# Kernel optimization log

Hardware: AMD Instinct MI355X
Metric: run time of the kernel (lower is better)

Reference implementation:

```python
import jax, jax.numpy as jnp
import numpy as np

DIM = 1024
HEADS = 16
DIM_HEAD = 64
SCALE = DIM_HEAD ** -0.5
LN_EPS = 1e-5


def layer_norm(x, g, b):
    mu = jnp.mean(x, axis=-1, keepdims=True)
    var = jnp.mean(jnp.square(x - mu), axis=-1, keepdims=True)
    return (x - mu) * jax.lax.rsqrt(var + LN_EPS) * g + b


def setup_inputs() -> dict:
    key = jax.random.key(0)
    ks = jax.random.split(key, 8)
    w_std = DIM ** -0.5  # keep GEMM outputs O(1)
    return {
        "query": jax.random.normal(ks[0], (4, 512, DIM), jnp.float32),
        "kv": jax.random.normal(ks[1], (4, 2048, DIM), jnp.float32),
        "ln_q_g": jnp.ones((DIM,), jnp.float32),
        "ln_q_b": jnp.zeros((DIM,), jnp.float32),
        "ln_kv_g": jnp.ones((DIM,), jnp.float32),
        "ln_kv_b": jnp.zeros((DIM,), jnp.float32),
        "Wq": jax.random.normal(ks[2], (DIM, DIM), jnp.float32) * w_std,
        "bq": jnp.zeros((DIM,), jnp.float32),
        "Wk": jax.random.normal(ks[3], (DIM, DIM), jnp.float32) * w_std,
        "bk": jnp.zeros((DIM,), jnp.float32),
        "Wv": jax.random.normal(ks[4], (DIM, DIM), jnp.float32) * w_std,
        "bv": jnp.zeros((DIM,), jnp.float32),
        "Wo": jax.random.normal(ks[5], (DIM, DIM), jnp.float32) * w_std,
        "bo": jnp.zeros((DIM,), jnp.float32),
    }


def reference(query, kv, ln_q_g, ln_q_b, ln_kv_g, ln_kv_b,
              Wq, bq, Wk, bk, Wv, bv, Wo, bo):
    kv_n = layer_norm(kv, ln_kv_g, ln_kv_b)            # (b, n_kv, d)
    residual = query
    q_n = layer_norm(query, ln_q_g, ln_q_b)            # (b, n_q, d)

    q = q_n @ Wq + bq                                   # (b, n_q, inner)
    kv_input = jnp.concatenate((kv_n, q_n), axis=-2)    # (b, n_kv+n_q, d)
    k = kv_input @ Wk + bk
    v = kv_input @ Wv + bv

    def split_heads(t):
        b, n, _ = t.shape
        return t.reshape(b, n, HEADS, DIM_HEAD).transpose(0, 2, 1, 3)  # b h n dh

    q = split_heads(q) * SCALE
    k = split_heads(k)
    v = split_heads(v)

    sim = jnp.einsum('bhid,bhjd->bhij', q, k)           # (b, h, n_q, n_kv+n_q)
    sim = sim - jax.lax.stop_gradient(jnp.max(sim, axis=-1, keepdims=True))
    attn = jax.nn.softmax(sim, axis=-1)
    out = jnp.einsum('bhij,bhjd->bhid', attn, v)        # (b, h, n_q, dh)

    b, h, n, dh = out.shape
    out = out.transpose(0, 2, 1, 3).reshape(b, n, h * dh)
    return out @ Wo + bo + residual
```

## Files before the change

### kernel.cpp

```cpp
#include <hip/hip_runtime.h>
#include <hip/hip_bf16.h>

#define B_    4
#define NQ    512
#define NKV   2048
#define NT    2560
#define DIM_  1024
#define HEADS 16
#define DH    64
#define NSEQT 10240
#define SCALE_Q_L2E 0.18033688011112042f

typedef short bf16x8 __attribute__((ext_vector_type(8)));
typedef float f32x4  __attribute__((ext_vector_type(4)));
typedef __hip_bfloat16 bf16;

__device__ inline void gll16(const bf16* g, bf16* l) {
  __builtin_amdgcn_global_load_lds(
      (const __attribute__((address_space(1))) unsigned int*)g,
      (__attribute__((address_space(3))) unsigned int*)l, 16, 0, 0);
}

__global__ __launch_bounds__(256) void prep_kernel(
    const float* __restrict__ query, const float* __restrict__ kv,
    const float* __restrict__ lgq, const float* __restrict__ lbq,
    const float* __restrict__ lgkv, const float* __restrict__ lbkv,
    bf16* __restrict__ X,
    const float* __restrict__ W0, const float* __restrict__ W1,
    const float* __restrict__ W2, const float* __restrict__ W3,
    bf16* __restrict__ T0, bf16* __restrict__ T1,
    bf16* __restrict__ T2, bf16* __restrict__ T3)
{
  __shared__ __align__(16) char psm[9216];
  const int t = threadIdx.x;
  const int blkid = blockIdx.x;
  if (blkid < B_*NT) {
    float* sh = (float*)psm;
    int b = blkid / NT, r = blkid % NT;
    const float *src, *g, *bb;
    if (r < NKV) { src = kv    + ((size_t)b*NKV + r)*DIM_;      g = lgkv; bb = lbkv; }
    else         { src = query + ((size_t)b*NQ + (r-NKV))*DIM_; g = lgq;  bb = lbq;  }
    float4 v = ((const float4*)src)[t];
    float s  = v.x+v.y+v.z+v.w;
    float s2 = v.x*v.x+v.y*v.y+v.z*v.z+v.w*v.w;
    #pragma unroll
    for (int m=1;m<64;m<<=1){ s += __shfl_xor(s,m,64); s2 += __shfl_xor(s2,m,64); }
    int wave=t>>6, lane=t&63;
    if(lane==0){ sh[wave]=s; sh[4+wave]=s2; }
    __syncthreads();
    s  = sh[0]+sh[1]+sh[2]+sh[3];
    s2 = sh[4]+sh[5]+sh[6]+sh[7];
    float mu = s*(1.0f/DIM_);
    float rs = rsqrtf(s2*(1.0f/DIM_) - mu*mu + 1e-5f);
    float4 gg = ((const float4*)g)[t];
    float4 b4 = ((const float4*)bb)[t];
    bf16* dst = X + (size_t)blkid*DIM_ + t*4;
    dst[0]=__float2bfloat16((v.x-mu)*rs*gg.x + b4.x);
    dst[1]=__float2bfloat16((v.y-mu)*rs*gg.y + b4.y);
    dst[2]=__float2bfloat16((v.z-mu)*rs*gg.z + b4.z);
    dst[3]=__float2bfloat16((v.w-mu)*rs*gg.w + b4.w);
  } else {
    int l = blkid - B_*NT;
    const float* W; bf16* Wt;
    switch (l>>8) {
      case 0: W=W0; Wt=T0; break;
      case 1: W=W1; Wt=T1; break;
      case 2: W=W2; Wt=T2; break;
      default: W=W3; Wt=T3; break;
    }
    int rem = l & 255;
    int k0 = (rem&15)*64, n0 = (rem>>4)*64;
    bf16* Ws = (bf16*)psm;
    int kr = t>>2, nseg = (t&3)*16;
    const float4* s4 = (const float4*)(W + (size_t)(k0+kr)*DIM_ + n0 + nseg);
    union { uint4 u[2]; bf16 h[16]; } pk;
    #pragma unroll
    for (int j=0;j<4;j++){
      float4 v = s4[j];
      pk.h[j*4+0]=__float2bfloat16(v.x); pk.h[j*4+1]=__float2bfloat16(v.y);
      pk.h[j*4+2]=__float2bfloat16(v.z); pk.h[j*4+3]=__float2bfloat16(v.w);
    }
    *(uint4*)(Ws + kr*72 + nseg)     = pk.u[0];
    *(uint4*)(Ws + kr*72 + nseg + 8) = pk.u[1];
    __syncthreads();
    int n = t&63, kseg = t>>6;
    union { uint4 u[2]; bf16 h[16]; } o;
    #pragma unroll
    for (int k=0;k<16;k++) o.h[k] = Ws[(kseg*16+k)*72 + n];
    bf16* dst = Wt + (size_t)(n0+n)*DIM_ + k0 + kseg*16;
    *(uint4*)dst = o.u[0];
    *(uint4*)(dst+8) = o.u[1];
  }
}

__device__ __forceinline__ void gemm_core(
    const bf16* __restrict__ A, const bf16* __restrict__ Bmat,
    const float* __restrict__ bias, const float* __restrict__ residual,
    void* __restrict__ outv, int rows_per_batch, int row_offset,
    int a_batch_stride_rows, int n_seq, float scale,
    int emode, int m0, int n0, char* smem)
{
  bf16* As = (bf16*)smem;
  bf16* Bs = (bf16*)(smem + 8192);
  float* Ts = (float*)smem;

  const int t = threadIdx.x;
  const int r0 = t>>2, c8 = (t&3)*8;
  int gm0 = m0 + r0, gm1 = m0 + 64 + r0;
  int b0i = gm0 / rows_per_batch, b1i = gm1 / rows_per_batch;
  const bf16* a0 = A + ((size_t)b0i*a_batch_stride_rows + row_offset + (gm0 - b0i*rows_per_batch))*(size_t)DIM_ + c8;
  const bf16* a1 = A + ((size_t)b1i*a_batch_stride_rows + row_offset + (gm1 - b1i*rows_per_batch))*(size_t)DIM_ + c8;
  const bf16* wb0 = Bmat + (size_t)(n0 + r0)*DIM_ + c8;
  const bf16* wb1 = Bmat + (size_t)(n0 + 64 + r0)*DIM_ + c8;
  bf16* lA0 = As + t*8;  bf16* lA1 = As + 64*32 + t*8;
  bf16* lB0 = Bs + t*8;  bf16* lB1 = Bs + 64*32 + t*8;

  const int wave = t>>6, lane = t&63, qq = lane>>4, mr = lane&15;
  const int wm = (wave>>1)*64, wn = (wave&1)*64;

  f32x4 acc[4][4] = {};
  for (int k0 = 0; k0 < DIM_; k0 += 32) {
    gll16(a0 + k0, lA0);
    gll16(a1 + k0, lA1);
    gll16(wb0 + k0, lB0);
    gll16(wb1 + k0, lB1);
    __syncthreads();
    bf16x8 af[4], bfr[4];
    #pragma unroll
    for (int ms=0;ms<4;ms++) af[ms]  = *(const bf16x8*)(As + (wm+ms*16+mr)*32 + qq*8);
    #pragma unroll
    for (int ns=0;ns<4;ns++) bfr[ns] = *(const bf16x8*)(Bs + (wn+ns*16+mr)*32 + qq*8);
    #pragma unroll
    for (int ms=0;ms<4;ms++)
      #pragma unroll
      for (int ns=0;ns<4;ns++)
        acc[ms][ns] = __builtin_amdgcn_mfma_f32_16x16x32_bf16(af[ms], bfr[ns], acc[ms][ns], 0,0,0);
    __syncthreads();
  }

  const int lr = t>>3, cs = (t&7)*16;
  for (int R=0; R<4; R++){
    if ((wave>>1) == (R>>1)) {
      #pragma unroll
      for (int ms2=0; ms2<2; ms2++){
        int ms = (R&1)*2 + ms2;
        #pragma unroll
        for (int ns=0; ns<4; ns++){
          int col = wn + ns*16 + mr;
          #pragma unroll
          for (int r=0;r<4;r++)
            Ts[(ms2*16 + qq*4 + r)*132 + col] = acc[ms][ns][r];
        }
      }
    }
    __syncthreads();
    float v[16];
    #pragma unroll
    for (int j=0;j<4;j++){
      float4 f = *(const float4*)(Ts + lr*132 + cs + j*4);
      v[j*4+0]=f.x; v[j*4+1]=f.y; v[j*4+2]=f.z; v[j*4+3]=f.w;
    }
    int gr = m0 + R*32 + lr;
    int gc = n0 + cs;
    if (emode == 0) {
      float* out = (float*)outv;
      size_t base = (size_t)gr*DIM_ + gc;
      #pragma unroll
      for (int j=0;j<4;j++){
        float4 bv = *(const float4*)(bias + gc + j*4);
        float4 rv = *(const float4*)(residual + base + j*4);
        float4 o4;
        o4.x = v[j*4+0] + bv.x + rv.x;
        o4.y = v[j*4+1] + bv.y + rv.y;
        o4.z = v[j*4+2] + bv.z + rv.z;
        o4.w = v[j*4+3] + bv.w + rv.w;
        *(float4*)(out + base + j*4) = o4;
      }
    } else if (emode == 1) {
      int bb = gr / rows_per_batch;
      int n  = gr - bb*rows_per_batch;
      int hh = gc>>6, dh = gc&63;
      bf16* out = (bf16*)outv + ((size_t)(bb*HEADS + hh)*n_seq + n)*DH + dh;
      union { uint4 u[2]; bf16 h[16]; } pk;
      #pragma unroll
      for (int j=0;j<16;j++) pk.h[j] = __float2bfloat16((v[j] + bias[gc+j])*scale);
      *(uint4*)out     = pk.u[0];
      *(uint4*)(out+8) = pk.u[1];
    } else {
      float bc = bias[gr];
      bf16* out = (bf16*)outv + (size_t)gr*NSEQT + gc;
      union { uint4 u[2]; bf16 h[16]; } pk;
      #pragma unroll
      for (int j=0;j<16;j++) pk.h[j] = __float2bfloat16(v[j] + bc);
      *(uint4*)out     = pk.u[0];
      *(uint4*)(out+8) = pk.u[1];
    }
    __syncthreads();
  }
}

__global__ __launch_bounds__(256) void gemm_qkv(
    const bf16* __restrict__ X,
    const bf16* __restrict__ WtQ, const bf16* __restrict__ WtK,
    const bf16* __restrict__ WtV,
    const float* __restrict__ bq, const float* __restrict__ bk,
    const float* __restrict__ bv,
    bf16* __restrict__ Qhb, bf16* __restrict__ Khb, bf16* __restrict__ VTg)
{
  __shared__ __align__(16) char smem[16896];
  const int blk = blockIdx.x;
  if (blk < 128) {
    gemm_core(X, WtQ, bq, nullptr, Qhb, NQ, NKV, NT, NQ, SCALE_Q_L2E, 1,
              (blk&15)*128, (blk>>4)*128, smem);
  } else if (blk < 768) {
    int l = blk - 128;
    gemm_core(X, WtK, bk, nullptr, Khb, NT, 0, NT, NT, 1.0f, 1,
              (l%80)*128, (l/80)*128, smem);
  } else {
    int l = blk - 768;
    gemm_core(WtV, X, bv, nullptr, VTg, DIM_, 0, DIM_, NSEQT, 1.0f, 2,
              (l/80)*128, (l%80)*128, smem);
  }
}

__global__ __launch_bounds__(256) void gemm_o(
    const bf16* __restrict__ Ctx, const bf16* __restrict__ WtO,
    const float* __restrict__ bo, const float* __restrict__ residual,
    float* __restrict__ out)
{
  __shared__ __align__(16) char smem[16896];
  const int blk = blockIdx.x;
  gemm_core(Ctx, WtO, bo, residual, out, B_*NQ, 0, B_*NQ, NQ, 1.0f, 0,
            (blk&15)*128, (blk>>4)*128, smem);
}

__global__ __launch_bounds__(256) void attn6_kernel(
    const bf16* __restrict__ Qh, const bf16* __restrict__ Kh,
    const bf16* __restrict__ VTg, bf16* __restrict__ Ctx)
{
  __shared__ __align__(16) bf16 KV[2][8192];
  __shared__ __align__(16) unsigned int Ps[4][640];

  const int t = threadIdx.x, wave = t>>6, lane = t&63;
  const int qq = lane>>4, mr = lane&15;
  const int blk = blockIdx.x;
  const int bh = (blk&7)*8 + (blk>>6);
  const int q0 = ((blk>>3)&7)*64;
  const int b = bh>>4, h = bh&15;
  const int pair = wave>>1, kh = wave&1;
  const int qb = pair*32;

  const int sl = t>>2, sc = t&3;
  const int skey = 32*(sl>>5) + 2*(sl&15) + ((sl>>4)&1);
  const bf16* Kb  = Kh + (size_t)bh*NT*DH + (size_t)skey*DH + sc*8;
  const bf16* VbT = VTg + ((size_t)(h*DH) + sl)*NSEQT + (size_t)b*NT + sc*8;

  bf16x8 qf[2][2];
  #pragma unroll
  for (int mt=0; mt<2; mt++){
    const bf16* Qb = Qh + ((size_t)bh*NQ + q0 + qb + mt*16 + mr)*DH;
    qf[mt][0] = *(const bf16x8*)(Qb + qq*8);
    qf[mt][1] = *(const bf16x8*)(Qb + 32 + qq*8);
  }

  f32x4 o[2][4] = {};
  float l[2][4] = {};
  unsigned int* Pw = &Ps[wave][0];

  {
    bf16* bp = &KV[0][0];
    gll16(Kb,        bp + t*8);
    gll16(Kb + 32,   bp + 2048 + t*8);
    gll16(VbT,       bp + 4096 + t*8);
    gll16(VbT + 32,  bp + 6144 + t*8);
  }

  for (int it = 0; it < NT/64; it++) {
    __syncthreads();
    if (it + 1 < NT/64) {
      int kt = (it+1)*64;
      bf16* bp = &KV[(it+1)&1][0];
      gll16(Kb  + (size_t)kt*DH,      bp + t*8);
      gll16(Kb  + (size_t)kt*DH + 32, bp + 2048 + t*8);
      gll16(VbT + kt,                 bp + 4096 + t*8);
      gll16(VbT + kt + 32,            bp + 6144 + t*8);
    }
    const bf16* cbuf = &KV[it&1][0];

    bf16x8 kf[2][2];
    #pragma unroll
    for (int g=0; g<2; g++){
      kf[g][0] = *(const bf16x8*)(cbuf + (32*kh + 16*g + mr)*32 + qq*8);
      kf[g][1] = *(const bf16x8*)(cbuf + 2048 + (32*kh + 16*g + mr)*32 + qq*8);
    }
    f32x4 s[2][2];
    #pragma unroll
    for (int mt=0; mt<2; mt++)
      #pragma unroll
      for (int g=0; g<2; g++){
        f32x4 z = {};
        z = __builtin_amdgcn_mfma_f32_16x16x32_bf16(qf[mt][0], kf[g][0], z, 0,0,0);
        z = __builtin_amdgcn_mfma_f32_16x16x32_bf16(qf[mt][1], kf[g][1], z, 0,0,0);
        s[mt][g] = z;
      }
    bf16x8 vf[4];
    #pragma unroll
    for (int n2=0; n2<4; n2++)
      vf[n2] = *(const bf16x8*)(cbuf + 4096 + kh*2048 + (n2*16+mr)*32 + qq*8);

    #pragma unroll
    for (int mt=0; mt<2; mt++)
      #pragma unroll
      for (int r=0; r<4; r++){
        float e0 = __builtin_amdgcn_exp2f(s[mt][0][r]);
        float e1 = __builtin_amdgcn_exp2f(s[mt][1][r]);
        l[mt][r] += e0 + e1;
        unsigned a0 = __float_as_uint(e0) + 0x8000u;
        unsigned a1 = __float_as_uint(e1) + 0x8000u;
        Pw[(mt*16 + qq*4 + r)*20 + mr] = __builtin_amdgcn_perm(a1, a0, 0x07060302u);
      }
    asm volatile("s_waitcnt lgkmcnt(0)" ::: "memory");
    bf16x8 pa[2];
    #pragma unroll
    for (int mt=0; mt<2; mt++)
      pa[mt] = *(const bf16x8*)(Pw + (mt*16+mr)*20 + qq*4);
    #pragma unroll
    for (int mt=0; mt<2; mt++)
      #pragma unroll
      for (int n2=0; n2<4; n2++)
        o[mt][n2] = __builtin_amdgcn_mfma_f32_16x16x32_bf16(pa[mt], vf[n2], o[mt][n2], 0,0,0);
  }

  float lsum[2][4];
  #pragma unroll
  for (int mt=0; mt<2; mt++)
    #pragma unroll
    for (int r=0; r<4; r++){
      float v = l[mt][r];
      #pragma unroll
      for (int m=1;m<16;m<<=1) v += __shfl_xor(v, m, 16);
      lsum[mt][r] = v;
    }

  __syncthreads();
  float* Of  = (float*)&KV[0][0];
  float* lsh = (float*)&Ps[0][0];
  if (kh == 1) {
    #pragma unroll
    for (int mt=0; mt<2; mt++){
      #pragma unroll
      for (int n2=0; n2<4; n2++)
        #pragma unroll
        for (int r=0; r<4; r++)
          Of[(qb + mt*16 + qq*4 + r)*68 + n2*16 + mr] = o[mt][n2][r];
      if (mr == 0)
        #pragma unroll
        for (int r=0; r<4; r++)
          lsh[qb + mt*16 + qq*4 + r] = lsum[mt][r];
    }
  }
  __syncthreads();
  if (kh == 0) {
    #pragma unroll
    for (int mt=0; mt<2; mt++)
      #pragma unroll
      for (int r=0; r<4; r++){
        int row = qb + mt*16 + qq*4 + r;
        float rl = 1.0f / (lsum[mt][r] + lsh[row]);
        #pragma unroll
        for (int n2=0; n2<4; n2++){
          int idx = row*68 + n2*16 + mr;
          Of[idx] = (o[mt][n2][r] + Of[idx]) * rl;
        }
      }
  }
  __syncthreads();
  {
    int row = t>>2, seg = (t&3)*16;
    union { uint4 u[2]; bf16 hh[16]; } pkv;
    #pragma unroll
    for (int j=0;j<16;j++) pkv.hh[j] = __float2bfloat16(Of[row*68 + seg + j]);
    bf16* dst = Ctx + ((size_t)b*NQ + q0 + row)*DIM_ + h*DH + seg;
    *(uint4*)dst = pkv.u[0];
    *(uint4*)(dst+8) = pkv.u[1];
  }
}

extern "C" void kernel_launch(void* const* d_in, const int* in_sizes, int n_in,
                              void* d_out, int out_size, void* d_ws, size_t ws_size,
                              hipStream_t stream)
{
  const float* query  = (const float*)d_in[0];
  const float* kv     = (const float*)d_in[1];
  const float* ln_q_g = (const float*)d_in[2];
  const float* ln_q_b = (const float*)d_in[3];
  const float* ln_kv_g= (const float*)d_in[4];
  const float* ln_kv_b= (const float*)d_in[5];
  const float* Wq = (const float*)d_in[6];
  const float* bq = (const float*)d_in[7];
  const float* Wk = (const float*)d_in[8];
  const float* bk = (const float*)d_in[9];
  const float* Wv = (const float*)d_in[10];
  const float* bv = (const float*)d_in[11];
  const float* Wo = (const float*)d_in[12];
  const float* bo = (const float*)d_in[13];
  float* out = (float*)d_out;

  char* ws = (char*)d_ws;
  size_t off = 0;
  auto take = [&](size_t bytes)->char* {
    char* p = ws + off; off += (bytes + 255) & ~(size_t)255; return p;
  };
  bf16* X    = (bf16*)take((size_t)B_*NT*DIM_*2);
  bf16* Qhb  = (bf16*)take((size_t)B_*NQ*DIM_*2);
  bf16* Khb  = (bf16*)take((size_t)B_*NT*DIM_*2);
  bf16* VTg  = (bf16*)take((size_t)DIM_*NSEQT*2);
  bf16* Ctx  = (bf16*)take((size_t)B_*NQ*DIM_*2);
  bf16* WtQ  = (bf16*)take((size_t)DIM_*DIM_*2);
  bf16* WtK  = (bf16*)take((size_t)DIM_*DIM_*2);
  bf16* WtV  = (bf16*)take((size_t)DIM_*DIM_*2);
  bf16* WtO  = (bf16*)take((size_t)DIM_*DIM_*2);

  prep_kernel<<<B_*NT + 1024, 256, 0, stream>>>(
      query, kv, ln_q_g, ln_q_b, ln_kv_g, ln_kv_b, X,
      Wq, Wk, Wv, Wo, WtQ, WtK, WtV, WtO);

  gemm_qkv<<<1408, 256, 0, stream>>>(X, WtQ, WtK, WtV, bq, bk, bv,
                                     Qhb, Khb, VTg);

  attn6_kernel<<<512, 256, 0, stream>>>(Qhb, Khb, VTg, Ctx);

  gemm_o<<<128, 256, 0, stream>>>(Ctx, WtO, bo, query, out);
}
```

Measured before the change: 271.7 us.

## Rewrite QKV GEMM with 256x256 tiles, 8 waves, and interleaved async LDS prefetch

Replaces the 128x128 QKV projection GEMM with a dedicated 512-thread kernel that computes 256x256 output tiles and double-buffers 128 KB of LDS. Global-to-LDS loads for the next K step are issued in chunks between MFMA groups, using explicit vmcnt waits, barriers and raised wave priority around the MFMAs. The goal is more operand reuse per byte loaded and better overlap of memory traffic with matrix math. In exchange the grid shrinks to 352 blocks, which may leave CUs underused, and the large LDS footprint limits occupancy.

```diff
diff --git a/kernel.cpp b/kernel.cpp
--- a/kernel.cpp
+++ b/kernel.cpp
@@ -20,6 +20,9 @@
       (const __attribute__((address_space(1))) unsigned int*)g,
       (__attribute__((address_space(3))) unsigned int*)l, 16, 0, 0);
 }
+
+#define SBAR() do { __builtin_amdgcn_s_barrier(); __builtin_amdgcn_sched_barrier(0); } while (0)
+#define VMCNT(n) asm volatile("s_waitcnt vmcnt(" #n ")" ::: "memory")
 
 __global__ __launch_bounds__(256) void prep_kernel(
     const float* __restrict__ query, const float* __restrict__ kv,
@@ -199,7 +202,22 @@
   }
 }
 
-__global__ __launch_bounds__(256) void gemm_qkv(
+#define MFMA8(mbase, nbase, BF)                                               \
+  do {                                                                        \
+    __builtin_amdgcn_s_setprio(1);                                            \
+    _Pragma("unroll")                                                         \
+    for (int ms = 0; ms < 4; ++ms)                                            \
+      _Pragma("unroll")                                                       \
+      for (int ns = 0; ns < 2; ++ns) {                                        \
+        acc[(mbase)+ms][(nbase)+ns] = __builtin_amdgcn_mfma_f32_16x16x32_bf16(\
+            af[ms][0], BF[ns][0], acc[(mbase)+ms][(nbase)+ns], 0,0,0);        \
+        acc[(mbase)+ms][(nbase)+ns] = __builtin_amdgcn_mfma_f32_16x16x32_bf16(\
+            af[ms][1], BF[ns][1], acc[(mbase)+ms][(nbase)+ns], 0,0,0);        \
+      }                                                                       \
+    __builtin_amdgcn_s_setprio(0);                                            \
+  } while (0)
+
+__global__ __launch_bounds__(512, 2) void gemm_qkv2(
     const bf16* __restrict__ X,
     const bf16* __restrict__ WtQ, const bf16* __restrict__ WtK,
     const bf16* __restrict__ WtV,
@@ -207,19 +225,165 @@
     const float* __restrict__ bv,
     bf16* __restrict__ Qhb, bf16* __restrict__ Khb, bf16* __restrict__ VTg)
 {
-  __shared__ __align__(16) char smem[16896];
+  __shared__ __align__(16) char smem[131072];
+  const int t   = threadIdx.x;
   const int blk = blockIdx.x;
-  if (blk < 128) {
-    gemm_core(X, WtQ, bq, nullptr, Qhb, NQ, NKV, NT, NQ, SCALE_Q_L2E, 1,
-              (blk&15)*128, (blk>>4)*128, smem);
-  } else if (blk < 768) {
-    int l = blk - 128;
-    gemm_core(X, WtK, bk, nullptr, Khb, NT, 0, NT, NT, 1.0f, 1,
-              (l%80)*128, (l/80)*128, smem);
+
+  const bf16 *A, *Bm; const float* bias; bf16* outp;
+  int m0, n0, amode, emode, npb, nseq; float scale;
+  if (blk < 32) {
+    A = X; Bm = WtQ; bias = bq; outp = Qhb;
+    m0 = (blk & 7) * 256; n0 = (blk >> 3) * 256;
+    amode = 1; emode = 1; npb = NQ; nseq = NQ; scale = SCALE_Q_L2E;
+  } else if (blk < 192) {
+    int l = blk - 32;
+    A = X; Bm = WtK; bias = bk; outp = Khb;
+    m0 = (l % 40) * 256; n0 = (l / 40) * 256;
+    amode = 0; emode = 1; npb = NT; nseq = NT; scale = 1.0f;
   } else {
-    int l = blk - 768;
-    gemm_core(WtV, X, bv, nullptr, VTg, DIM_, 0, DIM_, NSEQT, 1.0f, 2,
-              (l/80)*128, (l%80)*128, smem);
+    int l = blk - 192;
+    A = WtV; Bm = X; bias = bv; outp = VTg;
+    m0 = (l / 40) * 256; n0 = (l % 40) * 256;
+    amode = 0; emode = 2; npb = DIM_; nseq = 1; scale = 1.0f;
+  }
+
+  const int srow = t >> 3;
+  const int gsw  = (t & 7) ^ (srow & 7);
+  const bf16* pA[4]; const bf16* pB[4];
+  #pragma unroll
+  for (int c = 0; c < 4; ++c) {
+    int gm = m0 + c*64 + srow;
+    int sr = amode ? ((gm >> 9) * NT + NKV + (gm & (NQ-1))) : gm;
+    pA[c] = A  + (size_t)sr * DIM_ + gsw * 8;
+    pB[c] = Bm + (size_t)(n0 + c*64 + srow) * DIM_ + gsw * 8;
+  }
+
+  const int wave = t >> 6, lane = t & 63;
+  const int qq = lane >> 4, mr = lane & 15;
+  const int wr = wave >> 2, wc = wave & 3;
+  const int xg0 = ( qq      ^ (mr & 7)) << 4;
+  const int xg1 = ((4 + qq) ^ (mr & 7)) << 4;
+  const int awb = (wr*128 + mr) * 128;
+  const int bwb = (wc*64  + mr) * 128;
+  char* const sA = smem;
+  char* const sB = smem + 65536;
+  const int toff = t * 16;
+
+  f32x4 acc[8][4] = {};
+
+  gll16(pB[0], (bf16*)(sB + 0*8192 + toff));
+  gll16(pB[1], (bf16*)(sB + 1*8192 + toff));
+  gll16(pB[2], (bf16*)(sB + 2*8192 + toff));
+  gll16(pB[3], (bf16*)(sB + 3*8192 + toff));
+  gll16(pA[0], (bf16*)(sA + 0*8192 + toff));
+  gll16(pA[2], (bf16*)(sA + 2*8192 + toff));
+  gll16(pA[1], (bf16*)(sA + 1*8192 + toff));
+  gll16(pA[3], (bf16*)(sA + 3*8192 + toff));
+  VMCNT(2);
+  SBAR();
+
+  for (int kt = 0; kt < 16; ++kt) {
+    char* AsB = sA + ((kt & 1) << 15);
+    char* BsB = sB + ((kt & 1) << 15);
+    char* AsN = sA + (((kt + 1) & 1) << 15);
+    char* BsN = sB + (((kt + 1) & 1) << 15);
+    const int kn = ((kt + 1) & 15) << 6;
+
+    bf16x8 af[4][2], bf0[2][2], bf1[2][2];
+
+    #pragma unroll
+    for (int ms = 0; ms < 4; ++ms) {
+      af[ms][0] = *(const bf16x8*)(AsB + awb + ms*2048 + xg0);
+      af[ms][1] = *(const bf16x8*)(AsB + awb + ms*2048 + xg1);
+    }
+    #pragma unroll
+    for (int ns = 0; ns < 2; ++ns) {
+      bf0[ns][0] = *(const bf16x8*)(BsB + bwb + ns*2048 + xg0);
+      bf0[ns][1] = *(const bf16x8*)(BsB + bwb + ns*2048 + xg1);
+    }
+    gll16(pB[0] + kn, (bf16*)(BsN + 0*8192 + toff));
+    gll16(pB[1] + kn, (bf16*)(BsN + 1*8192 + toff));
+    SBAR();
+    MFMA8(0, 0, bf0);
+    SBAR();
+
+    #pragma unroll
+    for (int ns = 0; ns < 2; ++ns) {
+      bf1[ns][0] = *(const bf16x8*)(BsB + bwb + (2+ns)*2048 + xg0);
+      bf1[ns][1] = *(const bf16x8*)(BsB + bwb + (2+ns)*2048 + xg1);
+    }
+    gll16(pB[2] + kn, (bf16*)(BsN + 2*8192 + toff));
+    gll16(pB[3] + kn, (bf16*)(BsN + 3*8192 + toff));
+    SBAR();
+    MFMA8(0, 2, bf1);
+    VMCNT(4);
+    SBAR();
+
+    #pragma unroll
+    for (int ms = 0; ms < 4; ++ms) {
+      af[ms][0] = *(const bf16x8*)(AsB + awb + (4+ms)*2048 + xg0);
+      af[ms][1] = *(const bf16x8*)(AsB + awb + (4+ms)*2048 + xg1);
+    }
+    gll16(pA[0] + kn, (bf16*)(AsN + 0*8192 + toff));
+    gll16(pA[2] + kn, (bf16*)(AsN + 2*8192 + toff));
+    SBAR();
+    MFMA8(4, 0, bf0);
+    SBAR();
+
+    gll16(pA[1] + kn, (bf16*)(AsN + 1*8192 + toff));
+    gll16(pA[3] + kn, (bf16*)(AsN + 3*8192 + toff));
+    SBAR();
+    MFMA8(4, 2, bf1);
+    VMCNT(2);
+    SBAR();
+  }
+
+  VMCNT(0);
+  __syncthreads();
+
+  float* Of = (float*)smem;
+  const int er = t >> 4, ec = (t & 15) * 16;
+  #pragma unroll
+  for (int R = 0; R < 8; ++R) {
+    if (wr == (R >> 2)) {
+      #pragma unroll
+      for (int j = 0; j < 2; ++j)
+        #pragma unroll
+        for (int nf = 0; nf < 4; ++nf)
+          #pragma unroll
+          for (int r = 0; r < 4; ++r)
+            Of[(j*16 + qq*4 + r)*264 + wc*64 + nf*16 + mr] = acc[((R&3)<<1)+j][nf][r];
+    }
+    __syncthreads();
+    {
+      int gr = m0 + R*32 + er;
+      int gc = n0 + ec;
+      float v[16];
+      #pragma unroll
+      for (int j = 0; j < 4; ++j) {
+        float4 f = *(const float4*)(Of + er*264 + ec + j*4);
+        v[j*4+0]=f.x; v[j*4+1]=f.y; v[j*4+2]=f.z; v[j*4+3]=f.w;
+      }
+      if (emode == 1) {
+        int bb = gr / npb, n = gr - bb*npb;
+        int hh = gc >> 6, dh = gc & 63;
+        bf16* o = outp + ((size_t)(bb*HEADS + hh)*nseq + n)*DH + dh;
+        union { uint4 u[2]; bf16 h[16]; } pk;
+        #pragma unroll
+        for (int j = 0; j < 16; ++j) pk.h[j] = __float2bfloat16((v[j] + bias[gc+j])*scale);
+        *(uint4*)o     = pk.u[0];
+        *(uint4*)(o+8) = pk.u[1];
+      } else {
+        float bc = bias[gr];
+        bf16* o = outp + (size_t)gr*NSEQT + gc;
+        union { uint4 u[2]; bf16 h[16]; } pk;
+        #pragma unroll
+        for (int j = 0; j < 16; ++j) pk.h[j] = __float2bfloat16(v[j] + bc);
+        *(uint4*)o     = pk.u[0];
+        *(uint4*)(o+8) = pk.u[1];
+      }
+    }
+    __syncthreads();
   }
 }
 
@@ -425,7 +589,7 @@
       query, kv, ln_q_g, ln_q_b, ln_kv_g, ln_kv_b, X,
       Wq, Wk, Wv, Wo, WtQ, WtK, WtV, WtO);
 
-  gemm_qkv<<<1408, 256, 0, stream>>>(X, WtQ, WtK, WtV, bq, bk, bv,
+  gemm_qkv2<<<352, 512, 0, stream>>>(X, WtQ, WtK, WtV, bq, bk, bv,
                                      Qhb, Khb, VTg);
 
   attn6_kernel<<<512, 256, 0, stream>>>(Qhb, Khb, VTg, Ctx);
```

Result: no change. 270.9 us (-0.3%).

## Double-buffer GEMM LDS tiles with BK=64, XOR swizzle and MFMA priority

Applied to the files above, without the earlier changes.

Rewrites the shared GEMM core used by the QKV and output projections. It now double-buffers LDS so the next K tile's global-to-LDS loads overlap the current tile's MFMAs, and it widens the K step from 32 to 64. An XOR swizzle on the 16-byte chunks avoids LDS bank conflicts, and s_setprio raises wave priority around the MFMA block. LDS per block grows from about 17KB to 64KB, which reduces how many blocks can be resident per CU.

```diff
diff --git a/kernel.cpp b/kernel.cpp
--- a/kernel.cpp
+++ b/kernel.cpp
@@ -20,6 +20,9 @@
       (const __attribute__((address_space(1))) unsigned int*)g,
       (__attribute__((address_space(3))) unsigned int*)l, 16, 0, 0);
 }
+
+#define VMCNT(n) asm volatile("s_waitcnt vmcnt(" #n ")" ::: "memory")
+#define BAR() __builtin_amdgcn_s_barrier()
 
 __global__ __launch_bounds__(256) void prep_kernel(
     const float* __restrict__ query, const float* __restrict__ kv,
@@ -93,50 +96,78 @@
   }
 }
 
-__device__ __forceinline__ void gemm_core(
+__device__ __forceinline__ void gemm_core2(
     const bf16* __restrict__ A, const bf16* __restrict__ Bmat,
     const float* __restrict__ bias, const float* __restrict__ residual,
     void* __restrict__ outv, int rows_per_batch, int row_offset,
     int a_batch_stride_rows, int n_seq, float scale,
     int emode, int m0, int n0, char* smem)
 {
-  bf16* As = (bf16*)smem;
-  bf16* Bs = (bf16*)(smem + 8192);
+  char* const sA = smem;
+  char* const sB = smem + 32768;
   float* Ts = (float*)smem;
 
   const int t = threadIdx.x;
-  const int r0 = t>>2, c8 = (t&3)*8;
-  int gm0 = m0 + r0, gm1 = m0 + 64 + r0;
-  int b0i = gm0 / rows_per_batch, b1i = gm1 / rows_per_batch;
-  const bf16* a0 = A + ((size_t)b0i*a_batch_stride_rows + row_offset + (gm0 - b0i*rows_per_batch))*(size_t)DIM_ + c8;
-  const bf16* a1 = A + ((size_t)b1i*a_batch_stride_rows + row_offset + (gm1 - b1i*rows_per_batch))*(size_t)DIM_ + c8;
-  const bf16* wb0 = Bmat + (size_t)(n0 + r0)*DIM_ + c8;
-  const bf16* wb1 = Bmat + (size_t)(n0 + 64 + r0)*DIM_ + c8;
-  bf16* lA0 = As + t*8;  bf16* lA1 = As + 64*32 + t*8;
-  bf16* lB0 = Bs + t*8;  bf16* lB1 = Bs + 64*32 + t*8;
+  const int srow = t >> 3;
+  const int gsw  = (t & 7) ^ (srow & 7);
+  const bf16* pA[4]; const bf16* pB[4];
+  #pragma unroll
+  for (int c = 0; c < 4; ++c) {
+    int gm = m0 + c*32 + srow;
+    int bi = gm / rows_per_batch;
+    pA[c] = A + ((size_t)bi*a_batch_stride_rows + row_offset
+                 + (gm - bi*rows_per_batch))*(size_t)DIM_ + gsw*8;
+    pB[c] = Bmat + (size_t)(n0 + c*32 + srow)*(size_t)DIM_ + gsw*8;
+  }
+  const int toff = t*16;
 
   const int wave = t>>6, lane = t&63, qq = lane>>4, mr = lane&15;
   const int wm = (wave>>1)*64, wn = (wave&1)*64;
+  const int xq0 = (( qq    ) ^ (mr&7)) << 4;
+  const int xq1 = ((4 + qq ) ^ (mr&7)) << 4;
 
   f32x4 acc[4][4] = {};
-  for (int k0 = 0; k0 < DIM_; k0 += 32) {
-    gll16(a0 + k0, lA0);
-    gll16(a1 + k0, lA1);
-    gll16(wb0 + k0, lB0);
-    gll16(wb1 + k0, lB1);
-    __syncthreads();
-    bf16x8 af[4], bfr[4];
-    #pragma unroll
-    for (int ms=0;ms<4;ms++) af[ms]  = *(const bf16x8*)(As + (wm+ms*16+mr)*32 + qq*8);
-    #pragma unroll
-    for (int ns=0;ns<4;ns++) bfr[ns] = *(const bf16x8*)(Bs + (wn+ns*16+mr)*32 + qq*8);
-    #pragma unroll
-    for (int ms=0;ms<4;ms++)
-      #pragma unroll
-      for (int ns=0;ns<4;ns++)
-        acc[ms][ns] = __builtin_amdgcn_mfma_f32_16x16x32_bf16(af[ms], bfr[ns], acc[ms][ns], 0,0,0);
-    __syncthreads();
-  }
+
+  #pragma unroll
+  for (int c=0;c<4;++c) gll16(pA[c], (bf16*)(sA + c*4096 + toff));
+  #pragma unroll
+  for (int c=0;c<4;++c) gll16(pB[c], (bf16*)(sB + c*4096 + toff));
+  VMCNT(0);
+  BAR();
+
+  for (int kt = 0; kt < 16; ++kt) {
+    const int cb = (kt&1) << 14;
+    const int nb = ((kt+1)&1) << 14;
+    if (kt < 15) {
+      const int ko = (kt+1)*64;
+      #pragma unroll
+      for (int c=0;c<4;++c) gll16(pA[c] + ko, (bf16*)(sA + nb + c*4096 + toff));
+      #pragma unroll
+      for (int c=0;c<4;++c) gll16(pB[c] + ko, (bf16*)(sB + nb + c*4096 + toff));
+    }
+    #pragma unroll
+    for (int kh = 0; kh < 2; ++kh) {
+      const int xq = kh ? xq1 : xq0;
+      bf16x8 af[4], bfr[4];
+      #pragma unroll
+      for (int ms=0; ms<4; ++ms)
+        af[ms]  = *(const bf16x8*)(sA + cb + (wm + ms*16 + mr)*128 + xq);
+      #pragma unroll
+      for (int ns=0; ns<4; ++ns)
+        bfr[ns] = *(const bf16x8*)(sB + cb + (wn + ns*16 + mr)*128 + xq);
+      __builtin_amdgcn_s_setprio(1);
+      #pragma unroll
+      for (int ms=0; ms<4; ++ms)
+        #pragma unroll
+        for (int ns=0; ns<4; ++ns)
+          acc[ms][ns] = __builtin_amdgcn_mfma_f32_16x16x32_bf16(
+              af[ms], bfr[ns], acc[ms][ns], 0,0,0);
+      __builtin_amdgcn_s_setprio(0);
+    }
+    VMCNT(0);
+    BAR();
+  }
+  __syncthreads();
 
   const int lr = t>>3, cs = (t&7)*16;
   for (int R=0; R<4; R++){
@@ -199,7 +230,7 @@
   }
 }
 
-__global__ __launch_bounds__(256) void gemm_qkv(
+__global__ __launch_bounds__(256) void gemm_qkv3(
     const bf16* __restrict__ X,
     const bf16* __restrict__ WtQ, const bf16* __restrict__ WtK,
     const bf16* __restrict__ WtV,
@@ -207,19 +238,19 @@
     const float* __restrict__ bv,
     bf16* __restrict__ Qhb, bf16* __restrict__ Khb, bf16* __restrict__ VTg)
 {
-  __shared__ __align__(16) char smem[16896];
+  __shared__ __align__(16) char smem[65536];
   const int blk = blockIdx.x;
   if (blk < 128) {
-    gemm_core(X, WtQ, bq, nullptr, Qhb, NQ, NKV, NT, NQ, SCALE_Q_L2E, 1,
-              (blk&15)*128, (blk>>4)*128, smem);
+    gemm_core2(X, WtQ, bq, nullptr, Qhb, NQ, NKV, NT, NQ, SCALE_Q_L2E, 1,
+               (blk&15)*128, (blk>>4)*128, smem);
   } else if (blk < 768) {
     int l = blk - 128;
-    gemm_core(X, WtK, bk, nullptr, Khb, NT, 0, NT, NT, 1.0f, 1,
-              (l%80)*128, (l/80)*128, smem);
+    gemm_core2(X, WtK, bk, nullptr, Khb, NT, 0, NT, NT, 1.0f, 1,
+               (l%80)*128, (l/80)*128, smem);
   } else {
     int l = blk - 768;
-    gemm_core(WtV, X, bv, nullptr, VTg, DIM_, 0, DIM_, NSEQT, 1.0f, 2,
-              (l/80)*128, (l%80)*128, smem);
+    gemm_core2(WtV, X, bv, nullptr, VTg, DIM_, 0, DIM_, NSEQT, 1.0f, 2,
+               (l/80)*128, (l%80)*128, smem);
   }
 }
 
@@ -228,10 +259,10 @@
     const float* __restrict__ bo, const float* __restrict__ residual,
     float* __restrict__ out)
 {
-  __shared__ __align__(16) char smem[16896];
+  __shared__ __align__(16) char smem[65536];
   const int blk = blockIdx.x;
-  gemm_core(Ctx, WtO, bo, residual, out, B_*NQ, 0, B_*NQ, NQ, 1.0f, 0,
-            (blk&15)*128, (blk>>4)*128, smem);
+  gemm_core2(Ctx, WtO, bo, residual, out, B_*NQ, 0, B_*NQ, NQ, 1.0f, 0,
+             (blk&15)*128, (blk>>4)*128, smem);
 }
 
 __global__ __launch_bounds__(256) void attn6_kernel(
@@ -425,8 +456,8 @@
       query, kv, ln_q_g, ln_q_b, ln_kv_g, ln_kv_b, X,
       Wq, Wk, Wv, Wo, WtQ, WtK, WtV, WtO);
 
-  gemm_qkv<<<1408, 256, 0, stream>>>(X, WtQ, WtK, WtV, bq, bk, bv,
-                                     Qhb, Khb, VTg);
+  gemm_qkv3<<<1408, 256, 0, stream>>>(X, WtQ, WtK, WtV, bq, bk, bv,
+                                      Qhb, Khb, VTg);
 
   attn6_kernel<<<512, 256, 0, stream>>>(Qhb, Khb, VTg, Ctx);
 
```

After: 234.0 us. 13.9% less time.
